# Kernel optimization log

Hardware: AMD Instinct MI355X
Metric: run time of the kernel (lower is better)

Reference implementation:

```python
import jax, jax.numpy as jnp
import numpy as np

NEG_SLOPE = 0.2  # PyG GATConv default negative_slope


def setup_inputs() -> dict:
    key = jax.random.key(0)
    k1, k2, k3, k4, k5, k6 = jax.random.split(key, 6)
    N, E, DIN, DOUT = 100000, 1600000, 128, 64
    x = jax.random.normal(k1, (N, DIN), dtype=jnp.float32)
    edge_index = jax.random.randint(k2, (2, E), 0, N, dtype=jnp.int64)
    # learned params (glorot-like scale)
    W = jax.random.normal(k3, (DIN, DOUT), dtype=jnp.float32) * (1.0 / np.sqrt(DIN))
    att_src = jax.random.normal(k4, (DOUT,), dtype=jnp.float32) * (1.0 / np.sqrt(DOUT))
    att_dst = jax.random.normal(k5, (DOUT,), dtype=jnp.float32) * (1.0 / np.sqrt(DOUT))
    bias = jnp.zeros((DOUT,), dtype=jnp.float32)
    return {"x": x, "edge_index": edge_index, "W": W,
            "att_src": att_src, "att_dst": att_dst, "bias": bias}


def reference(x, edge_index, W, att_src, att_dst, bias):
    N = x.shape[0]
    # add self loops (PyG default add_self_loops=True)
    loop = jnp.arange(N, dtype=edge_index.dtype)
    src = jnp.concatenate([edge_index[0], loop])  # message sources (x_j)
    dst = jnp.concatenate([edge_index[1], loop])  # aggregation targets (x_i)

    h = x @ W                         # [N, C] linear transform (heads=1)
    a_src = h @ att_src               # [N] per-node source score
    a_dst = h @ att_dst               # [N] per-node target score

    # per-edge raw attention: LeakyReLU(alpha_j + alpha_i)
    e = jax.nn.leaky_relu(a_src[src] + a_dst[dst], NEG_SLOPE)  # [Etot]

    # segment softmax over edges grouped by destination node
    e_max = jax.ops.segment_max(e, dst, num_segments=N)        # every node has self loop
    e_exp = jnp.exp(e - e_max[dst])
    e_sum = jax.ops.segment_sum(e_exp, dst, num_segments=N)
    alpha = e_exp / (e_sum[dst] + 1e-16)                       # [Etot]

    # weighted scatter-add aggregation
    out = jax.ops.segment_sum(h[src] * alpha[:, None], dst, num_segments=N)
    return out + bias
```

## Files before the change

kernel.cpp:

```cpp
#include <hip/hip_runtime.h>
#include <cstddef>

#define DIN 128
#define DOUT 64
#define BKT_SHIFT 7
#define BKT_NODES 128
#define CAP 2680
#define CAPP 2816
#define MAXB 800
#define EPB 8192
#define TW 784

#define QDEC (0.25f / 32767.f)
#define QENC (32767.f / 0.25f)

typedef __attribute__((ext_vector_type(8))) short bf16x8;
typedef __attribute__((ext_vector_type(4))) float f32x4;

__device__ __forceinline__ float leakyrelu(float v) { return v > 0.f ? v : 0.2f * v; }

__device__ __forceinline__ unsigned cvtpk(float lo, float hi) {
    unsigned r;
    asm volatile("v_cvt_pk_bf16_f32 %0, %1, %2" : "=v"(r) : "v"(lo), "v"(hi));
    return r;
}
__device__ __forceinline__ bf16x8 cvt8(f32x4 lo, f32x4 hi) {
    union { bf16x8 v; unsigned u[4]; } cv;
    cv.u[0] = cvtpk(lo[0], lo[1]);
    cv.u[1] = cvtpk(lo[2], lo[3]);
    cv.u[2] = cvtpk(hi[0], hi[1]);
    cv.u[3] = cvtpk(hi[2], hi[3]);
    return cv.v;
}

__global__ __launch_bounds__(1024) void k_front(
    const float* __restrict__ x, const float* __restrict__ W,
    const float* __restrict__ att_src, const float* __restrict__ att_dst,
    signed char* __restrict__ h8, float2* __restrict__ sa2, float* __restrict__ adst,
    const int* __restrict__ src, const int* __restrict__ dst,
    unsigned int* __restrict__ sorted, int* __restrict__ table,
    int N, int E, int NB, int NBT)
{
    __shared__ unsigned int sbufL[EPB];
    __shared__ int hist[MAXB];
    __shared__ int offA[MAXB + 1];
    const int tid = threadIdx.x;

    if (blockIdx.x < NBT) {
        const int lane = tid & 63, g = lane >> 4, c15 = lane & 15;
        const int n0w = blockIdx.x * 512 + (tid >> 6) * 32;
        if (n0w >= N) return;

        bf16x8 afrag[2][4];
        #pragma unroll
        for (int u = 0; u < 2; ++u) {
            const int arow = min(n0w + u * 16 + c15, N - 1);
            const float* xr = x + (size_t)arow * DIN + g * 8;
            #pragma unroll
            for (int kb = 0; kb < 4; ++kb) {
                f32x4 lo = *reinterpret_cast<const f32x4*>(xr + kb * 32);
                f32x4 hi = *reinterpret_cast<const f32x4*>(xr + kb * 32 + 4);
                afrag[u][kb] = cvt8(lo, hi);
            }
        }

        f32x4 acc[2][4];
        #pragma unroll
        for (int nt = 0; nt < 4; ++nt) {
            f32x4 a0 = {0.f, 0.f, 0.f, 0.f};
            f32x4 a1 = {0.f, 0.f, 0.f, 0.f};
            #pragma unroll
            for (int kb = 0; kb < 4; ++kb) {
                const float* wp = W + (size_t)(kb * 32 + g * 8) * DOUT + nt * 16 + c15;
                f32x4 lo, hi;
                #pragma unroll
                for (int i = 0; i < 4; ++i) lo[i] = wp[i * DOUT];
                #pragma unroll
                for (int i = 0; i < 4; ++i) hi[i] = wp[(i + 4) * DOUT];
                bf16x8 bfr = cvt8(lo, hi);
                a0 = __builtin_amdgcn_mfma_f32_16x16x32_bf16(afrag[0][kb], bfr, a0, 0, 0, 0);
                a1 = __builtin_amdgcn_mfma_f32_16x16x32_bf16(afrag[1][kb], bfr, a1, 0, 0, 0);
            }
            acc[0][nt] = a0;
            acc[1][nt] = a1;
        }

        #pragma unroll
        for (int u = 0; u < 2; ++u) {
            float mr[4];
            #pragma unroll
            for (int r = 0; r < 4; ++r) {
                float m = fabsf(acc[u][0][r]);
                #pragma unroll
                for (int nt = 1; nt < 4; ++nt) m = fmaxf(m, fabsf(acc[u][nt][r]));
                mr[r] = m;
            }
            #pragma unroll
            for (int mask = 1; mask < 16; mask <<= 1)
                #pragma unroll
                for (int r = 0; r < 4; ++r) mr[r] = fmaxf(mr[r], __shfl_xor(mr[r], mask));

            float inv[4];
            #pragma unroll
            for (int r = 0; r < 4; ++r) inv[r] = 127.f / fmaxf(mr[r], 1e-20f);

            #pragma unroll
            for (int nt = 0; nt < 4; ++nt)
                #pragma unroll
                for (int r = 0; r < 4; ++r) {
                    int row = n0w + u * 16 + g * 4 + r;
                    if (row < N) {
                        int qi = __float2int_rn(acc[u][nt][r] * inv[r]);
                        qi = max(-127, min(127, qi));
                        h8[(size_t)row * DOUT + nt * 16 + c15] = (signed char)qi;
                    }
                }

            float ps[4] = {0.f, 0.f, 0.f, 0.f}, pd[4] = {0.f, 0.f, 0.f, 0.f};
            #pragma unroll
            for (int nt = 0; nt < 4; ++nt) {
                float as = att_src[nt * 16 + c15];
                float ad = att_dst[nt * 16 + c15];
                #pragma unroll
                for (int r = 0; r < 4; ++r) {
                    ps[r] = fmaf(acc[u][nt][r], as, ps[r]);
                    pd[r] = fmaf(acc[u][nt][r], ad, pd[r]);
                }
            }
            #pragma unroll
            for (int mask = 1; mask < 16; mask <<= 1)
                #pragma unroll
                for (int r = 0; r < 4; ++r) {
                    ps[r] += __shfl_xor(ps[r], mask);
                    pd[r] += __shfl_xor(pd[r], mask);
                }
            #pragma unroll
            for (int r = 0; r < 4; ++r) {
                int row = n0w + u * 16 + g * 4 + r;
                if (c15 == r && row < N) {
                    sa2[row] = make_float2(ps[r], fmaxf(mr[r], 1e-20f) * (1.f / 127.f));
                    adst[row] = pd[r];
                }
            }
        }
        return;
    }

    const int c = blockIdx.x - NBT;
    const int e0 = c * EPB;
    const int cnt = min(EPB, E - e0);

    for (int i = tid; i < NB; i += 1024) hist[i] = 0;
    __syncthreads();

    unsigned pv[8]; int bv[8], rv[8];
    #pragma unroll
    for (int k = 0; k < 8; ++k) {
        int e = e0 + k * 1024 + tid;
        if (e < E) {
            int d = dst[e];
            pv[k] = (unsigned)src[e] | ((unsigned)(d & (BKT_NODES - 1)) << 17);
            bv[k] = d >> BKT_SHIFT;
            rv[k] = atomicAdd(&hist[bv[k]], 1);
        } else bv[k] = -1;
    }
    __syncthreads();

    if (tid < NB) offA[tid + 1] = hist[tid];
    if (tid == 0) offA[0] = 0;
    __syncthreads();
    for (int st = 1; st < NB; st <<= 1) {
        int add = 0;
        if (tid < NB && tid >= st) add = offA[tid + 1 - st];
        __syncthreads();
        if (tid < NB && tid >= st) offA[tid + 1] += add;
        __syncthreads();
    }

    for (int i = tid; i <= NB; i += 1024) table[(size_t)c * TW + i] = offA[i];

    #pragma unroll
    for (int k = 0; k < 8; ++k)
        if (bv[k] >= 0) sbufL[offA[bv[k]] + rv[k]] = pv[k];
    __syncthreads();

    for (int i = tid; i < cnt; i += 1024)
        sorted[(size_t)c * EPB + i] = sbufL[i];
}

__global__ __launch_bounds__(512) void k_csr(
    const unsigned int* __restrict__ sorted, const int* __restrict__ table,
    const float2* __restrict__ sa2, const float* __restrict__ adst,
    unsigned int* __restrict__ cpk, int2* __restrict__ nspan,
    int N, int NC)
{
    __shared__ unsigned int el[CAP];
    __shared__ float eal[CAP];
    __shared__ int cpre[513];
    __shared__ int hist[BKT_NODES], hist2[BKT_NODES], offs[BKT_NODES + 1];
    __shared__ float ssumL[BKT_NODES], selfC[BKT_NODES], adL[BKT_NODES];

    const int tid = threadIdx.x;
    const int b = blockIdx.x;
    const int n0 = b << BKT_SHIFT;
    const int nn = min(BKT_NODES, N - n0);

    int s0 = 0, len = 0;
    if (tid < NC) {
        s0 = table[(size_t)tid * TW + b];
        len = table[(size_t)tid * TW + b + 1] - s0;
    }
    if (tid < NC) cpre[tid + 1] = len;
    if (tid == 0) cpre[0] = 0;
    __syncthreads();
    for (int st = 1; st < NC; st <<= 1) {
        int add = 0;
        if (tid < NC && tid >= st) add = cpre[tid + 1 - st];
        __syncthreads();
        if (tid < NC && tid >= st) cpre[tid + 1] += add;
        __syncthreads();
    }
    if (tid < NC && len > 0) {
        int d0 = cpre[tid];
        const unsigned int* p = sorted + (size_t)tid * EPB + s0;
        int lim = min(len, CAP - d0);
        for (int i = 0; i < lim; ++i) el[d0 + i] = p[i];
    }
    if (tid < BKT_NODES) { hist[tid] = 0; hist2[tid] = 0; }
    if (tid < nn) {
        int n = n0 + tid;
        float ad = adst[n];
        adL[tid] = ad;
        float2 v = sa2[n];
        float selfA = __expf(leakyrelu(v.x + ad));
        ssumL[tid] = selfA;
        selfC[tid] = selfA * v.y;
    }
    __syncthreads();
    int cnt = cpre[NC]; if (cnt > CAP) cnt = CAP;

    for (int i = tid; i < cnt; i += 512) {
        unsigned int e = el[i];
        int ln = e >> 17;
        float2 vs = sa2[e & 0x1FFFF];
        float a = __expf(leakyrelu(vs.x + adL[ln]));
        eal[i] = a * vs.y;
        atomicAdd(&hist[ln], 1);
        atomicAdd(&ssumL[ln], a);
    }
    __syncthreads();
    if (tid < nn) ssumL[tid] = 1.f / (ssumL[tid] + 1e-16f);

    if (tid < BKT_NODES) offs[tid + 1] = hist[tid] + 1;
    if (tid == 0) offs[0] = 0;
    __syncthreads();
    for (int off = 1; off < BKT_NODES; off <<= 1) {
        int v = 0;
        if (tid < BKT_NODES && tid >= off) v = offs[tid + 1 - off];
        __syncthreads();
        if (tid < BKT_NODES && tid >= off) offs[tid + 1] += v;
        __syncthreads();
    }

    const size_t gbase = (size_t)b * CAPP;
    for (int i = tid; i < cnt; i += 512) {
        unsigned int e = el[i];
        int ln = e >> 17;
        unsigned int s = e & 0x1FFFF;
        int r = atomicAdd(&hist2[ln], 1);
        int p = offs[ln] + r;
        float c = eal[i] * ssumL[ln];
        unsigned q = (unsigned)fminf(c * QENC + 0.5f, 32767.f);
        cpk[gbase + p] = s | (q << 17);
    }
    __syncthreads();

    if (tid < nn) {
        int n = n0 + tid;
        int pend = offs[tid + 1];
        float c = selfC[tid] * ssumL[tid];
        unsigned q = (unsigned)fminf(c * QENC + 0.5f, 32767.f);
        cpk[gbase + pend - 1] = (unsigned)n | (q << 17);
        nspan[n] = make_int2((int)gbase + offs[tid], (int)gbase + pend);
    }
}

__global__ __launch_bounds__(256) void k_agg(
    const int2* __restrict__ nspan, const unsigned int* __restrict__ cpk,
    const signed char* __restrict__ h8, const float* __restrict__ bias,
    float* __restrict__ out, int N)
{
    const int lane = threadIdx.x & 63;
    const int n = blockIdx.x * 4 + (threadIdx.x >> 6);
    if (n >= N) return;
    const int2 span = nspan[n];
    const int st = __builtin_amdgcn_readfirstlane(span.x);
    const int en = __builtin_amdgcn_readfirstlane(span.y);

    int acc0 = 0, acc1 = 0, acc2 = 0, acc3 = 0;
    int j = st;
    for (; j + 16 <= en; j += 16) {
        unsigned md[16]; int hv[16];
        #pragma unroll
        for (int q = 0; q < 16; ++q) md[q] = cpk[j + q];
        #pragma unroll
        for (int q = 0; q < 16; ++q)
            hv[q] = (int)h8[(size_t)(md[q] & 0x1FFFF) * DOUT + lane];
        #pragma unroll
        for (int q = 0; q < 16; q += 4) {
            acc0 += __mul24((int)(md[q + 0] >> 17), hv[q + 0]);
            acc1 += __mul24((int)(md[q + 1] >> 17), hv[q + 1]);
            acc2 += __mul24((int)(md[q + 2] >> 17), hv[q + 2]);
            acc3 += __mul24((int)(md[q + 3] >> 17), hv[q + 3]);
        }
    }
    if (j + 8 <= en) {
        unsigned md[8]; int hv[8];
        #pragma unroll
        for (int q = 0; q < 8; ++q) md[q] = cpk[j + q];
        #pragma unroll
        for (int q = 0; q < 8; ++q)
            hv[q] = (int)h8[(size_t)(md[q] & 0x1FFFF) * DOUT + lane];
        #pragma unroll
        for (int q = 0; q < 8; q += 4) {
            acc0 += __mul24((int)(md[q + 0] >> 17), hv[q + 0]);
            acc1 += __mul24((int)(md[q + 1] >> 17), hv[q + 1]);
            acc2 += __mul24((int)(md[q + 2] >> 17), hv[q + 2]);
            acc3 += __mul24((int)(md[q + 3] >> 17), hv[q + 3]);
        }
        j += 8;
    }
    if (j + 4 <= en) {
        unsigned md[4]; int hv[4];
        #pragma unroll
        for (int q = 0; q < 4; ++q) md[q] = cpk[j + q];
        #pragma unroll
        for (int q = 0; q < 4; ++q)
            hv[q] = (int)h8[(size_t)(md[q] & 0x1FFFF) * DOUT + lane];
        acc0 += __mul24((int)(md[0] >> 17), hv[0]);
        acc1 += __mul24((int)(md[1] >> 17), hv[1]);
        acc2 += __mul24((int)(md[2] >> 17), hv[2]);
        acc3 += __mul24((int)(md[3] >> 17), hv[3]);
        j += 4;
    }
    for (; j < en; ++j) {
        unsigned md = cpk[j];
        acc0 += __mul24((int)(md >> 17), (int)h8[(size_t)(md & 0x1FFFF) * DOUT + lane]);
    }

    float r = (float)((acc0 + acc1) + (acc2 + acc3)) * QDEC + bias[lane];
    __builtin_nontemporal_store(r, &out[(size_t)n * DOUT + lane]);
}

extern "C" void kernel_launch(void* const* d_in, const int* in_sizes, int n_in,
                              void* d_out, int out_size, void* d_ws, size_t ws_size,
                              hipStream_t stream)
{
    const float* x       = (const float*)d_in[0];
    const int*   edge    = (const int*)d_in[1];
    const float* W       = (const float*)d_in[2];
    const float* att_src = (const float*)d_in[3];
    const float* att_dst = (const float*)d_in[4];
    const float* bias    = (const float*)d_in[5];

    const int N = in_sizes[0] / DIN;
    const int E = in_sizes[1] / 2;
    const int* src = edge;
    const int* dst = edge + E;
    float* out = (float*)d_out;

    const int NB = (N + BKT_NODES - 1) >> BKT_SHIFT;
    const int NC = (E + EPB - 1) / EPB;
    const int NBT = (N + 511) / 512;

    signed char* h8 = (signed char*)d_ws;
    float2* sa2 = (float2*)(h8 + (size_t)N * DOUT);
    float* adst = (float*)(sa2 + N);
    int2* nspan = (int2*)(adst + N);
    unsigned int* sorted = (unsigned int*)(nspan + N);
    int* table = (int*)(sorted + (size_t)NC * EPB);
    unsigned int* cpk = (unsigned int*)(table + (size_t)NC * TW);

    k_front<<<NBT + NC, 1024, 0, stream>>>(x, W, att_src, att_dst, h8, sa2, adst,
                                           src, dst, sorted, table, N, E, NB, NBT);
    k_csr  <<<NB, 512, 0, stream>>>(sorted, table, sa2, adst, cpk, nspan, N, NC);
    k_agg  <<<(N + 3) / 4, 256, 0, stream>>>(nspan, cpk, h8, bias, out, N);
}
```

Measured before the change: 97.06 us.

## Split wavefront into four edge groups with 4-byte row gathers in aggregation

The aggregation kernel now maps 16 lanes per edge, each lane loading 4 int8 features as one 32-bit word, so a wavefront handles four edges at once. Edge metadata is loaded cooperatively, 32 entries at a time, and broadcast with shuffles. Partial sums are reduced across the four groups with xor-shuffles, and the result is written as float4. This is meant to cut the number of gather instructions and memory requests per edge, at the cost of shuffle overhead, masked tail work and narrower stores.

```diff
diff --git a/kernel.cpp b/kernel.cpp
--- a/kernel.cpp
+++ b/kernel.cpp
@@ -291,65 +291,52 @@
     float* __restrict__ out, int N)
 {
     const int lane = threadIdx.x & 63;
+    const int c15 = lane & 15;
+    const int grp = lane >> 4;
     const int n = blockIdx.x * 4 + (threadIdx.x >> 6);
     if (n >= N) return;
     const int2 span = nspan[n];
-    const int st = __builtin_amdgcn_readfirstlane(span.x);
-    const int en = __builtin_amdgcn_readfirstlane(span.y);
+    const int st = span.x, en = span.y;
+
+    const float4 bv = *reinterpret_cast<const float4*>(bias + c15 * 4);
 
     int acc0 = 0, acc1 = 0, acc2 = 0, acc3 = 0;
-    int j = st;
-    for (; j + 16 <= en; j += 16) {
-        unsigned md[16]; int hv[16];
-        #pragma unroll
-        for (int q = 0; q < 16; ++q) md[q] = cpk[j + q];
-        #pragma unroll
-        for (int q = 0; q < 16; ++q)
-            hv[q] = (int)h8[(size_t)(md[q] & 0x1FFFF) * DOUT + lane];
-        #pragma unroll
-        for (int q = 0; q < 16; q += 4) {
-            acc0 += __mul24((int)(md[q + 0] >> 17), hv[q + 0]);
-            acc1 += __mul24((int)(md[q + 1] >> 17), hv[q + 1]);
-            acc2 += __mul24((int)(md[q + 2] >> 17), hv[q + 2]);
-            acc3 += __mul24((int)(md[q + 3] >> 17), hv[q + 3]);
-        }
-    }
-    if (j + 8 <= en) {
-        unsigned md[8]; int hv[8];
-        #pragma unroll
-        for (int q = 0; q < 8; ++q) md[q] = cpk[j + q];
-        #pragma unroll
-        for (int q = 0; q < 8; ++q)
-            hv[q] = (int)h8[(size_t)(md[q] & 0x1FFFF) * DOUT + lane];
-        #pragma unroll
-        for (int q = 0; q < 8; q += 4) {
-            acc0 += __mul24((int)(md[q + 0] >> 17), hv[q + 0]);
-            acc1 += __mul24((int)(md[q + 1] >> 17), hv[q + 1]);
-            acc2 += __mul24((int)(md[q + 2] >> 17), hv[q + 2]);
-            acc3 += __mul24((int)(md[q + 3] >> 17), hv[q + 3]);
-        }
-        j += 8;
-    }
-    if (j + 4 <= en) {
-        unsigned md[4]; int hv[4];
-        #pragma unroll
-        for (int q = 0; q < 4; ++q) md[q] = cpk[j + q];
-        #pragma unroll
-        for (int q = 0; q < 4; ++q)
-            hv[q] = (int)h8[(size_t)(md[q] & 0x1FFFF) * DOUT + lane];
-        acc0 += __mul24((int)(md[0] >> 17), hv[0]);
-        acc1 += __mul24((int)(md[1] >> 17), hv[1]);
-        acc2 += __mul24((int)(md[2] >> 17), hv[2]);
-        acc3 += __mul24((int)(md[3] >> 17), hv[3]);
-        j += 4;
-    }
-    for (; j < en; ++j) {
-        unsigned md = cpk[j];
-        acc0 += __mul24((int)(md >> 17), (int)h8[(size_t)(md & 0x1FFFF) * DOUT + lane]);
-    }
-
-    float r = (float)((acc0 + acc1) + (acc2 + acc3)) * QDEC + bias[lane];
-    __builtin_nontemporal_store(r, &out[(size_t)n * DOUT + lane]);
+    for (int base = st; base < en; base += 32) {
+        unsigned mdl = cpk[min(base + (lane & 31), en - 1)];
+        unsigned mdq[8]; int qv[8]; unsigned hw[8];
+        #pragma unroll
+        for (int t = 0; t < 8; ++t) mdq[t] = __shfl(mdl, t * 4 + grp);
+        #pragma unroll
+        for (int t = 0; t < 8; ++t) {
+            int e = base + t * 4 + grp;
+            qv[t] = (e < en) ? (int)(mdq[t] >> 17) : 0;
+        }
+        #pragma unroll
+        for (int t = 0; t < 8; ++t)
+            hw[t] = *reinterpret_cast<const unsigned*>(
+                h8 + (size_t)(mdq[t] & 0x1FFFFu) * DOUT + c15 * 4);
+        #pragma unroll
+        for (int t = 0; t < 8; ++t) {
+            acc0 += __mul24(qv[t], (int)(signed char)(hw[t]));
+            acc1 += __mul24(qv[t], (int)(signed char)(hw[t] >> 8));
+            acc2 += __mul24(qv[t], (int)(signed char)(hw[t] >> 16));
+            acc3 += __mul24(qv[t], (int)(signed char)(hw[t] >> 24));
+        }
+    }
+
+    acc0 += __shfl_xor(acc0, 16); acc0 += __shfl_xor(acc0, 32);
+    acc1 += __shfl_xor(acc1, 16); acc1 += __shfl_xor(acc1, 32);
+    acc2 += __shfl_xor(acc2, 16); acc2 += __shfl_xor(acc2, 32);
+    acc3 += __shfl_xor(acc3, 16); acc3 += __shfl_xor(acc3, 32);
+
+    if (grp == 0) {
+        float4 r;
+        r.x = (float)acc0 * QDEC + bv.x;
+        r.y = (float)acc1 * QDEC + bv.y;
+        r.z = (float)acc2 * QDEC + bv.z;
+        r.w = (float)acc3 * QDEC + bv.w;
+        *reinterpret_cast<float4*>(out + (size_t)n * DOUT + c15 * 4) = r;
+    }
 }
 
 extern "C" void kernel_launch(void* const* d_in, const int* in_sizes, int n_in,
```

Measured after the change: 87.20 us. -10.2%, faster.
